# Optimization experiments

Hardware: AMD Instinct MI355X
Metric: run time of the kernel (lower is better)

Reference implementation:

```python
import jax, jax.numpy as jnp
import numpy as np

B, S, HID = 2, 2048, 1024
NH, HD = 16, 64  # num heads, head dim
NEG = 1e10

def setup_inputs() -> dict:
    key = jax.random.key(0)
    ks = jax.random.split(key, 4)
    scale = 1.0 / np.sqrt(HID)
    return {
        "hidden_states": jax.random.normal(ks[0], (B, S, HID), jnp.float32),
        "attention_mask": jnp.zeros((B, 1, 1, S), jnp.float32),
        "Wq": jax.random.normal(ks[1], (HID, HID), jnp.float32) * scale,
        "bq": jnp.zeros((HID,), jnp.float32),
        "Wk": jax.random.normal(ks[2], (HID, HID), jnp.float32) * scale,
        "bk": jnp.zeros((HID,), jnp.float32),
        "Wv": jax.random.normal(ks[3], (HID, HID), jnp.float32) * scale,
        "bv": jnp.zeros((HID,), jnp.float32),
    }

def _split_heads(x):
    # [B,S,HID] -> [B,NH,S,HD]
    return x.reshape(B, S, NH, HD).transpose(0, 2, 1, 3)

def reference(hidden_states, attention_mask, Wq, bq, Wk, bk, Wv, bv):
    q = _split_heads(hidden_states @ Wq.T + bq)
    k = _split_heads(hidden_states @ Wk.T + bk)
    v = _split_heads(hidden_states @ Wv.T + bv)
    scores = jnp.einsum("bhqd,bhkd->bhqk", q, k) / np.sqrt(HD)
    causal = jnp.tril(jnp.ones((S, S), jnp.float32))  # [S,S]
    scores = scores * causal - NEG * (1.0 - causal)
    scores = scores + attention_mask
    probs = jax.nn.softmax(scores, axis=-1)  # [B,NH,S,S]
    ctx = jnp.einsum("bhqk,bhkd->bhqd", probs, v)
    ctx = ctx.transpose(0, 2, 1, 3).reshape(B, S, HID)
    return (ctx, probs)
```

## Files before the change

kernel.cpp:

```cpp
#include <hip/hip_runtime.h>

#define S_LEN 2048
#define HIDN  1024
#define NHEAD 16
#define HDIM  64
#define NBATCH 2

typedef __bf16 bf16x8 __attribute__((ext_vector_type(8)));
typedef float  f32x4  __attribute__((ext_vector_type(4)));
typedef unsigned int  u32x4 __attribute__((ext_vector_type(4)));
typedef unsigned short u16;
typedef unsigned short u16x4 __attribute__((ext_vector_type(4)));

__device__ __forceinline__ u16 f2bf(float f) {
    union { float f; unsigned int u; } v; v.f = f;
    unsigned int u = v.u;
    unsigned int r = ((u >> 16) & 1u) + 0x7FFFu;
    return (u16)((u + r) >> 16);
}

__device__ __forceinline__ f32x4 mfma16(bf16x8 a, bf16x8 b, f32x4 c) {
    return __builtin_amdgcn_mfma_f32_16x16x32_bf16(a, b, c, 0, 0, 0);
}

__device__ __forceinline__ f32x4 zf4() { f32x4 z = {0.f, 0.f, 0.f, 0.f}; return z; }

__device__ __forceinline__ bf16x8 pack8_trunc(f32x4 a, f32x4 b) {
    union { f32x4 f; u32x4 u; } ua, ub;
    ua.f = a; ub.f = b;
    union { unsigned int d[4]; bf16x8 v; } r;
    r.d[0] = __builtin_amdgcn_perm(ua.u.y, ua.u.x, 0x07060302u);
    r.d[1] = __builtin_amdgcn_perm(ua.u.w, ua.u.z, 0x07060302u);
    r.d[2] = __builtin_amdgcn_perm(ub.u.y, ub.u.x, 0x07060302u);
    r.d[3] = __builtin_amdgcn_perm(ub.u.w, ub.u.z, 0x07060302u);
    return r.v;
}

__device__ __forceinline__ void gld16(void* lds, const void* g) {
    __builtin_amdgcn_global_load_lds(
        (const __attribute__((address_space(1))) void*)g,
        (__attribute__((address_space(3))) void*)lds, 16, 0, 0);
}

__global__ __launch_bounds__(256) void cvt_bf16(
    const float* __restrict__ s, u16* __restrict__ d, int n)
{
    int i = (blockIdx.x * 256 + threadIdx.x) * 4;
    if (i >= n) return;
    float4 v = *(const float4*)&s[i];
    u16x4 o = { f2bf(v.x), f2bf(v.y), f2bf(v.z), f2bf(v.w) };
    *(u16x4*)&d[i] = o;
}

__global__ __launch_bounds__(256) void qkv_gemm(
    const u16* __restrict__ hsb,
    const u16* __restrict__ Wqb, const u16* __restrict__ Wkb, const u16* __restrict__ Wvb,
    const float* __restrict__ bq, const float* __restrict__ bk, const float* __restrict__ bv,
    u16* __restrict__ Qf, u16* __restrict__ Kf, u16* __restrict__ Vt)
{
    __shared__ u16 As[128 * 32];
    __shared__ u16 Bs[128 * 32];

    const int z = blockIdx.z;
    const u16*   __restrict__ W    = (z == 0) ? Wqb : (z == 1) ? Wkb : Wvb;
    const float* __restrict__ bias = (z == 0) ? bq  : (z == 1) ? bk  : bv;

    const int mbase = blockIdx.x * 128;
    const int nbase = blockIdx.y * 128;
    const int tid  = threadIdx.x;
    const int lane = tid & 63;
    const int wv   = tid >> 6;
    const int wrow = wv >> 1, wcol = wv & 1;
    const int lrow = lane & 15, quad = lane >> 4;

    const int c0 = tid, c1 = tid + 256;
    const int r0 = c0 >> 2, o0 = (c0 & 3) * 8;
    const int r1 = c1 >> 2, o1 = (c1 & 3) * 8;
    const u16* a0p = &hsb[(size_t)(mbase + r0) * HIDN + o0];
    const u16* a1p = &hsb[(size_t)(mbase + r1) * HIDN + o1];
    const u16* b0p = &W  [(size_t)(nbase + r0) * HIDN + o0];
    const u16* b1p = &W  [(size_t)(nbase + r1) * HIDN + o1];

    f32x4 acc[4][4];
#pragma unroll
    for (int i = 0; i < 4; ++i)
#pragma unroll
        for (int j = 0; j < 4; ++j) acc[i][j] = zf4();

    for (int k0 = 0; k0 < HIDN; k0 += 32) {
        gld16(&As[c0 * 8], a0p + k0);
        gld16(&As[c1 * 8], a1p + k0);
        gld16(&Bs[c0 * 8], b0p + k0);
        gld16(&Bs[c1 * 8], b1p + k0);
        __syncthreads();

        bf16x8 af[4], bfr[4];
#pragma unroll
        for (int i = 0; i < 4; ++i)
            af[i] = *(const bf16x8*)&As[(wrow * 64 + i * 16 + lrow) * 32 + quad * 8];
#pragma unroll
        for (int j = 0; j < 4; ++j)
            bfr[j] = *(const bf16x8*)&Bs[(wcol * 64 + j * 16 + lrow) * 32 + quad * 8];
#pragma unroll
        for (int i = 0; i < 4; ++i)
#pragma unroll
            for (int j = 0; j < 4; ++j)
                acc[i][j] = mfma16(af[i], bfr[j], acc[i][j]);
        __syncthreads();
    }

    if (z == 2) {
        const int bb = mbase >> 11;
        const int sb = mbase & 2047;
#pragma unroll
        for (int i = 0; i < 4; ++i) {
#pragma unroll
            for (int j = 0; j < 4; ++j) {
                const int n = nbase + wcol * 64 + j * 16 + lrow;
                const int hh = n >> 6, d = n & 63;
                const float bs = bias[n];
                const int sbase = sb + wrow * 64 + i * 16 + quad * 4;
                u16x4 pk = { f2bf(acc[i][j][0] + bs), f2bf(acc[i][j][1] + bs),
                             f2bf(acc[i][j][2] + bs), f2bf(acc[i][j][3] + bs) };
                *(u16x4*)&Vt[(((size_t)(bb * NHEAD + hh)) * HDIM + d) * S_LEN + sbase] = pk;
            }
        }
    } else {
        u16* __restrict__ O = (z == 0) ? Qf : Kf;
#pragma unroll
        for (int i = 0; i < 4; ++i) {
#pragma unroll
            for (int j = 0; j < 4; ++j) {
                const int n = nbase + wcol * 64 + j * 16 + lrow;
                const float bs = bias[n];
#pragma unroll
                for (int reg = 0; reg < 4; ++reg) {
                    const int m = mbase + wrow * 64 + i * 16 + quad * 4 + reg;
                    O[(size_t)m * HIDN + n] = f2bf(acc[i][j][reg] + bs);
                }
            }
        }
    }
}

__global__ __launch_bounds__(256) void attn_kernel(
    const u16* __restrict__ Qf,
    const u16* __restrict__ Kf,
    const u16* __restrict__ Vt,
    const float* __restrict__ amask,
    float* __restrict__ ctx,
    float* __restrict__ probs)
{
    const int qt = 127 - blockIdx.x;
    const int h  = blockIdx.y;
    const int b  = blockIdx.z;
    const int bh = b * NHEAD + h;
    const int tid  = threadIdx.x;
    const int lane = tid & 63;
    const int wv   = tid >> 6;
    const int lrow = lane & 15, quad = lane >> 4;
    const int row0 = qt * 16;
    const int dti  = qt >> 2;
    const int nkt  = dti + 1;

    __shared__ float pfl[4][16 * 64];
    __shared__ float cxs[4][64 * 17];
    __shared__ float l_sh[4][16];

    {
        const int tail  = nkt * 64;
        const int nt4   = (S_LEN - tail) >> 2;
        const int r  = tid >> 4;
        const int c0 = tid & 15;
        const f32x4 zf = {0.f, 0.f, 0.f, 0.f};
        float* pr = &probs[((size_t)bh * S_LEN + row0 + r) * S_LEN + tail];
        for (int c4 = c0; c4 < nt4; c4 += 16)
            __builtin_nontemporal_store(zf, (f32x4*)&pr[c4 * 4]);
    }

    const u16* qp = &Qf[((size_t)b * S_LEN + row0 + lrow) * HIDN + h * HDIM + quad * 8];
    const bf16x8 qa0 = *(const bf16x8*)qp;
    const bf16x8 qa1 = *(const bf16x8*)(qp + 32);

    float l_lane[4] = {0.f, 0.f, 0.f, 0.f};
    for (int kt = wv; kt < nkt; kt += 4) {
        f32x4 c[4];
#pragma unroll
        for (int cb = 0; cb < 4; ++cb) {
            const int col = kt * 64 + cb * 16 + lrow;
            const u16* kp = &Kf[((size_t)b * S_LEN + col) * HIDN + h * HDIM + quad * 8];
            bf16x8 kb0 = *(const bf16x8*)kp;
            bf16x8 kb1 = *(const bf16x8*)(kp + 32);
            c[cb] = mfma16(qa0, kb0, zf4());
            c[cb] = mfma16(qa1, kb1, c[cb]);
        }
        if (kt == dti) {
#pragma unroll
            for (int cb = 0; cb < 4; ++cb) {
                const int col = kt * 64 + cb * 16 + lrow;
                const float m8 = amask[b * S_LEN + col] - 8.0f;
#pragma unroll
                for (int reg = 0; reg < 4; ++reg) {
                    const int row = row0 + quad * 4 + reg;
                    const float e = __expf(fmaf(c[cb][reg], 0.125f, m8));
                    l_lane[reg] += (col <= row) ? e : 0.f;
                }
            }
        } else {
#pragma unroll
            for (int cb = 0; cb < 4; ++cb) {
                const int col = kt * 64 + cb * 16 + lrow;
                const float m8 = amask[b * S_LEN + col] - 8.0f;
#pragma unroll
                for (int reg = 0; reg < 4; ++reg)
                    l_lane[reg] += __expf(fmaf(c[cb][reg], 0.125f, m8));
            }
        }
    }
#pragma unroll
    for (int reg = 0; reg < 4; ++reg) {
#pragma unroll
        for (int off = 1; off < 16; off <<= 1)
            l_lane[reg] += __shfl_xor(l_lane[reg], off, 16);
    }
    if (lrow == 0) {
#pragma unroll
        for (int reg = 0; reg < 4; ++reg)
            l_sh[wv][quad * 4 + reg] = l_lane[reg];
    }
    __syncthreads();
    float inv_l[4];
#pragma unroll
    for (int reg = 0; reg < 4; ++reg) {
        const int rr = quad * 4 + reg;
        inv_l[reg] = 1.f / (l_sh[0][rr] + l_sh[1][rr] + l_sh[2][rr] + l_sh[3][rr]);
    }

    f32x4 av[4];
#pragma unroll
    for (int db = 0; db < 4; ++db) av[db] = zf4();

    for (int kt = wv; kt < nkt; kt += 4) {
        f32x4 c[4];
#pragma unroll
        for (int cb = 0; cb < 4; ++cb) {
            const int col = kt * 64 + cb * 16 + lrow;
            const u16* kp = &Kf[((size_t)b * S_LEN + col) * HIDN + h * HDIM + quad * 8];
            bf16x8 kb0 = *(const bf16x8*)kp;
            bf16x8 kb1 = *(const bf16x8*)(kp + 32);
            c[cb] = mfma16(qa0, kb0, zf4());
            c[cb] = mfma16(qa1, kb1, c[cb]);
        }
        if (kt == dti) {
#pragma unroll
            for (int cb = 0; cb < 4; ++cb) {
                const int col = kt * 64 + cb * 16 + lrow;
                const float m8 = amask[b * S_LEN + col] - 8.0f;
#pragma unroll
                for (int reg = 0; reg < 4; ++reg) {
                    const int row = row0 + quad * 4 + reg;
                    const float p = (col <= row)
                        ? __expf(fmaf(c[cb][reg], 0.125f, m8)) * inv_l[reg] : 0.f;
                    pfl[wv][(quad * 4 + reg) * 64 + cb * 16 + lrow] = p;
                }
            }
        } else {
#pragma unroll
            for (int cb = 0; cb < 4; ++cb) {
                const int col = kt * 64 + cb * 16 + lrow;
                const float m8 = amask[b * S_LEN + col] - 8.0f;
#pragma unroll
                for (int reg = 0; reg < 4; ++reg) {
                    const float p = __expf(fmaf(c[cb][reg], 0.125f, m8)) * inv_l[reg];
                    pfl[wv][(quad * 4 + reg) * 64 + cb * 16 + lrow] = p;
                }
            }
        }

#pragma unroll
        for (int it = 0; it < 4; ++it) {
            const int r  = it * 4 + quad;
            const int f4 = lrow;
            f32x4 v = *(const f32x4*)&pfl[wv][r * 64 + f4 * 4];
            __builtin_nontemporal_store(
                v, (f32x4*)&probs[((size_t)bh * S_LEN + row0 + r) * S_LEN + kt * 64 + f4 * 4]);
        }

        f32x4 p0 = *(const f32x4*)&pfl[wv][lrow * 64 + quad * 8];
        f32x4 p1 = *(const f32x4*)&pfl[wv][lrow * 64 + quad * 8 + 4];
        f32x4 p2 = *(const f32x4*)&pfl[wv][lrow * 64 + 32 + quad * 8];
        f32x4 p3 = *(const f32x4*)&pfl[wv][lrow * 64 + 32 + quad * 8 + 4];
        bf16x8 pa0 = pack8_trunc(p0, p1);
        bf16x8 pa1 = pack8_trunc(p2, p3);
#pragma unroll
        for (int db = 0; db < 4; ++db) {
            const u16* vp = &Vt[((size_t)bh * HDIM + db * 16 + lrow) * S_LEN + kt * 64 + quad * 8];
            bf16x8 vb0 = *(const bf16x8*)vp;
            bf16x8 vb1 = *(const bf16x8*)(vp + 32);
            av[db] = mfma16(pa0, vb0, av[db]);
            av[db] = mfma16(pa1, vb1, av[db]);
        }
    }

#pragma unroll
    for (int db = 0; db < 4; ++db)
#pragma unroll
        for (int reg = 0; reg < 4; ++reg)
            cxs[wv][lane * 17 + db * 4 + reg] = av[db][reg];
    __syncthreads();
#pragma unroll
    for (int reg = 0; reg < 4; ++reg) {
        const int idx = lane * 17 + wv * 4 + reg;
        const float s = cxs[0][idx] + cxs[1][idx] + cxs[2][idx] + cxs[3][idx];
        __builtin_nontemporal_store(
            s, &ctx[((size_t)b * S_LEN + row0 + quad * 4 + reg) * HIDN + h * HDIM + wv * 16 + lrow]);
    }
}

extern "C" void kernel_launch(void* const* d_in, const int* in_sizes, int n_in,
                              void* d_out, int out_size, void* d_ws, size_t ws_size,
                              hipStream_t stream)
{
    const float* hs    = (const float*)d_in[0];
    const float* amask = (const float*)d_in[1];
    const float* Wq    = (const float*)d_in[2];
    const float* bq    = (const float*)d_in[3];
    const float* Wk    = (const float*)d_in[4];
    const float* bk    = (const float*)d_in[5];
    const float* Wv    = (const float*)d_in[6];
    const float* bv    = (const float*)d_in[7];

    float* out   = (float*)d_out;
    float* ctx   = out;
    float* probs = out + (size_t)NBATCH * S_LEN * HIDN;

    const size_t NTOK = (size_t)NBATCH * S_LEN;
    u16* hsb = (u16*)d_ws;
    u16* Wqb = hsb + NTOK * HIDN;
    u16* Wkb = Wqb + (size_t)HIDN * HIDN;
    u16* Wvb = Wkb + (size_t)HIDN * HIDN;
    u16* Qf  = Wvb + (size_t)HIDN * HIDN;
    u16* Kf  = Qf + NTOK * HIDN;
    u16* Vt  = Kf + NTOK * HIDN;

    const int n_hs = (int)(NTOK * HIDN);
    const int n_w  = HIDN * HIDN;
    cvt_bf16<<<n_hs / 1024, 256, 0, stream>>>(hs, hsb, n_hs);
    cvt_bf16<<<n_w  / 1024, 256, 0, stream>>>(Wq, Wqb, n_w);
    cvt_bf16<<<n_w  / 1024, 256, 0, stream>>>(Wk, Wkb, n_w);
    cvt_bf16<<<n_w  / 1024, 256, 0, stream>>>(Wv, Wvb, n_w);

    qkv_gemm<<<dim3(32, 8, 3), 256, 0, stream>>>(hsb, Wqb, Wkb, Wvb, bq, bk, bv, Qf, Kf, Vt);
    attn_kernel<<<dim3(128, 16, 2), 256, 0, stream>>>(Qf, Kf, Vt, amask, ctx, probs);
}
```

Before: 778.3 us.

## Give each wave its own 16-row query tile over all key tiles, dropping cross-wave reduction

The attention block now covers 64 query rows, with each of the 4 waves owning 16 rows and looping over every key tile. Before, 4 waves split the key tiles of one 16-row tile. This removes the shared-memory row-sum and context reductions and both __syncthreads, and cuts the grid from 128 to 32 blocks per head. The exponentials also switch to exp2f with log2e folded into the scale constants. The trade-offs are fewer blocks, uneven per-wave work, and waves reading the same K/V tiles separately instead of sharing them.

```diff
diff --git a/kernel.cpp b/kernel.cpp
--- a/kernel.cpp
+++ b/kernel.cpp
@@ -11,6 +11,10 @@
 typedef unsigned int  u32x4 __attribute__((ext_vector_type(4)));
 typedef unsigned short u16;
 typedef unsigned short u16x4 __attribute__((ext_vector_type(4)));
+
+#define LOG2E      1.4426950408889634f
+#define QS_L2E     0.18033688011112042f
+#define NEG8_L2E  -11.541560327111707f
 
 __device__ __forceinline__ u16 f2bf(float f) {
     union { float f; unsigned int u; } v; v.f = f;
@@ -151,7 +155,7 @@
     float* __restrict__ ctx,
     float* __restrict__ probs)
 {
-    const int qt = 127 - blockIdx.x;
+    const int qt = 31 - blockIdx.x;
     const int h  = blockIdx.y;
     const int b  = blockIdx.z;
     const int bh = b * NHEAD + h;
@@ -159,22 +163,19 @@
     const int lane = tid & 63;
     const int wv   = tid >> 6;
     const int lrow = lane & 15, quad = lane >> 4;
-    const int row0 = qt * 16;
-    const int dti  = qt >> 2;
-    const int nkt  = dti + 1;
+    const int nkt  = qt + 1;
+    const int row0 = qt * 64 + wv * 16;
 
     __shared__ float pfl[4][16 * 64];
-    __shared__ float cxs[4][64 * 17];
-    __shared__ float l_sh[4][16];
 
     {
-        const int tail  = nkt * 64;
-        const int nt4   = (S_LEN - tail) >> 2;
-        const int r  = tid >> 4;
-        const int c0 = tid & 15;
+        const int tail = nkt * 64;
+        const int nt4  = (S_LEN - tail) >> 2;
+        const int r  = tid >> 2;
+        const int c0 = tid & 3;
         const f32x4 zf = {0.f, 0.f, 0.f, 0.f};
-        float* pr = &probs[((size_t)bh * S_LEN + row0 + r) * S_LEN + tail];
-        for (int c4 = c0; c4 < nt4; c4 += 16)
+        float* pr = &probs[((size_t)bh * S_LEN + qt * 64 + r) * S_LEN + tail];
+        for (int c4 = c0; c4 < nt4; c4 += 4)
             __builtin_nontemporal_store(zf, (f32x4*)&pr[c4 * 4]);
     }
 
@@ -182,27 +183,30 @@
     const bf16x8 qa0 = *(const bf16x8*)qp;
     const bf16x8 qa1 = *(const bf16x8*)(qp + 32);
 
+    const float* __restrict__ am = &amask[(size_t)b * S_LEN];
+    const u16* __restrict__ kbase = &Kf[(size_t)b * S_LEN * HIDN + h * HDIM + quad * 8];
+
     float l_lane[4] = {0.f, 0.f, 0.f, 0.f};
-    for (int kt = wv; kt < nkt; kt += 4) {
+    for (int kt = 0; kt < nkt; ++kt) {
         f32x4 c[4];
 #pragma unroll
         for (int cb = 0; cb < 4; ++cb) {
             const int col = kt * 64 + cb * 16 + lrow;
-            const u16* kp = &Kf[((size_t)b * S_LEN + col) * HIDN + h * HDIM + quad * 8];
+            const u16* kp = kbase + (size_t)col * HIDN;
             bf16x8 kb0 = *(const bf16x8*)kp;
             bf16x8 kb1 = *(const bf16x8*)(kp + 32);
             c[cb] = mfma16(qa0, kb0, zf4());
             c[cb] = mfma16(qa1, kb1, c[cb]);
         }
-        if (kt == dti) {
+        if (kt == qt) {
 #pragma unroll
             for (int cb = 0; cb < 4; ++cb) {
                 const int col = kt * 64 + cb * 16 + lrow;
-                const float m8 = amask[b * S_LEN + col] - 8.0f;
+                const float m8 = fmaf(am[col], LOG2E, NEG8_L2E);
 #pragma unroll
                 for (int reg = 0; reg < 4; ++reg) {
                     const int row = row0 + quad * 4 + reg;
-                    const float e = __expf(fmaf(c[cb][reg], 0.125f, m8));
+                    const float e = exp2f(fmaf(c[cb][reg], QS_L2E, m8));
                     l_lane[reg] += (col <= row) ? e : 0.f;
                 }
             }
@@ -210,91 +214,83 @@
 #pragma unroll
             for (int cb = 0; cb < 4; ++cb) {
                 const int col = kt * 64 + cb * 16 + lrow;
-                const float m8 = amask[b * S_LEN + col] - 8.0f;
+                const float m8 = fmaf(am[col], LOG2E, NEG8_L2E);
 #pragma unroll
                 for (int reg = 0; reg < 4; ++reg)
-                    l_lane[reg] += __expf(fmaf(c[cb][reg], 0.125f, m8));
-            }
-        }
-    }
+                    l_lane[reg] += exp2f(fmaf(c[cb][reg], QS_L2E, m8));
+            }
+        }
+    }
+    float inv_l[4];
 #pragma unroll
     for (int reg = 0; reg < 4; ++reg) {
 #pragma unroll
         for (int off = 1; off < 16; off <<= 1)
             l_lane[reg] += __shfl_xor(l_lane[reg], off, 16);
-    }
-    if (lrow == 0) {
-#pragma unroll
-        for (int reg = 0; reg < 4; ++reg)
-            l_sh[wv][quad * 4 + reg] = l_lane[reg];
-    }
-    __syncthreads();
-    float inv_l[4];
-#pragma unroll
-    for (int reg = 0; reg < 4; ++reg) {
-        const int rr = quad * 4 + reg;
-        inv_l[reg] = 1.f / (l_sh[0][rr] + l_sh[1][rr] + l_sh[2][rr] + l_sh[3][rr]);
+        inv_l[reg] = 1.f / l_lane[reg];
     }
 
     f32x4 av[4];
 #pragma unroll
     for (int db = 0; db < 4; ++db) av[db] = zf4();
 
-    for (int kt = wv; kt < nkt; kt += 4) {
+    float* __restrict__ pw = pfl[wv];
+    const u16* __restrict__ vbase = &Vt[(size_t)bh * HDIM * S_LEN + quad * 8];
+
+    for (int kt = 0; kt < nkt; ++kt) {
         f32x4 c[4];
 #pragma unroll
         for (int cb = 0; cb < 4; ++cb) {
             const int col = kt * 64 + cb * 16 + lrow;
-            const u16* kp = &Kf[((size_t)b * S_LEN + col) * HIDN + h * HDIM + quad * 8];
+            const u16* kp = kbase + (size_t)col * HIDN;
             bf16x8 kb0 = *(const bf16x8*)kp;
             bf16x8 kb1 = *(const bf16x8*)(kp + 32);
             c[cb] = mfma16(qa0, kb0, zf4());
             c[cb] = mfma16(qa1, kb1, c[cb]);
         }
-        if (kt == dti) {
+        if (kt == qt) {
 #pragma unroll
             for (int cb = 0; cb < 4; ++cb) {
                 const int col = kt * 64 + cb * 16 + lrow;
-                const float m8 = amask[b * S_LEN + col] - 8.0f;
+                const float m8 = fmaf(am[col], LOG2E, NEG8_L2E);
 #pragma unroll
                 for (int reg = 0; reg < 4; ++reg) {
                     const int row = row0 + quad * 4 + reg;
                     const float p = (col <= row)
-                        ? __expf(fmaf(c[cb][reg], 0.125f, m8)) * inv_l[reg] : 0.f;
-                    pfl[wv][(quad * 4 + reg) * 64 + cb * 16 + lrow] = p;
+                        ? exp2f(fmaf(c[cb][reg], QS_L2E, m8)) * inv_l[reg] : 0.f;
+                    pw[(quad * 4 + reg) * 64 + cb * 16 + lrow] = p;
                 }
             }
         } else {
 #pragma unroll
             for (int cb = 0; cb < 4; ++cb) {
                 const int col = kt * 64 + cb * 16 + lrow;
-                const float m8 = amask[b * S_LEN + col] - 8.0f;
+                const float m8 = fmaf(am[col], LOG2E, NEG8_L2E);
 #pragma unroll
                 for (int reg = 0; reg < 4; ++reg) {
-                    const float p = __expf(fmaf(c[cb][reg], 0.125f, m8)) * inv_l[reg];
-                    pfl[wv][(quad * 4 + reg) * 64 + cb * 16 + lrow] = p;
+                    const float p = exp2f(fmaf(c[cb][reg], QS_L2E, m8)) * inv_l[reg];
+                    pw[(quad * 4 + reg) * 64 + cb * 16 + lrow] = p;
                 }
             }
         }
 
 #pragma unroll
         for (int it = 0; it < 4; ++it) {
-            const int r  = it * 4 + quad;
-            const int f4 = lrow;
-            f32x4 v = *(const f32x4*)&pfl[wv][r * 64 + f4 * 4];
+            const int r = it * 4 + quad;
+            f32x4 v = *(const f32x4*)&pw[r * 64 + lrow * 4];
             __builtin_nontemporal_store(
-                v, (f32x4*)&probs[((size_t)bh * S_LEN + row0 + r) * S_LEN + kt * 64 + f4 * 4]);
-        }
-
-        f32x4 p0 = *(const f32x4*)&pfl[wv][lrow * 64 + quad * 8];
-        f32x4 p1 = *(const f32x4*)&pfl[wv][lrow * 64 + quad * 8 + 4];
-        f32x4 p2 = *(const f32x4*)&pfl[wv][lrow * 64 + 32 + quad * 8];
-        f32x4 p3 = *(const f32x4*)&pfl[wv][lrow * 64 + 32 + quad * 8 + 4];
+                v, (f32x4*)&probs[((size_t)bh * S_LEN + row0 + r) * S_LEN + kt * 64 + lrow * 4]);
+        }
+
+        f32x4 p0 = *(const f32x4*)&pw[lrow * 64 + quad * 8];
+        f32x4 p1 = *(const f32x4*)&pw[lrow * 64 + quad * 8 + 4];
+        f32x4 p2 = *(const f32x4*)&pw[lrow * 64 + 32 + quad * 8];
+        f32x4 p3 = *(const f32x4*)&pw[lrow * 64 + 32 + quad * 8 + 4];
         bf16x8 pa0 = pack8_trunc(p0, p1);
         bf16x8 pa1 = pack8_trunc(p2, p3);
 #pragma unroll
         for (int db = 0; db < 4; ++db) {
-            const u16* vp = &Vt[((size_t)bh * HDIM + db * 16 + lrow) * S_LEN + kt * 64 + quad * 8];
+            const u16* vp = vbase + (size_t)(db * 16 + lrow) * S_LEN + kt * 64;
             bf16x8 vb0 = *(const bf16x8*)vp;
             bf16x8 vb1 = *(const bf16x8*)(vp + 32);
             av[db] = mfma16(pa0, vb0, av[db]);
@@ -303,17 +299,14 @@
     }
 
 #pragma unroll
-    for (int db = 0; db < 4; ++db)
-#pragma unroll
-        for (int reg = 0; reg < 4; ++reg)
-            cxs[wv][lane * 17 + db * 4 + reg] = av[db][reg];
-    __syncthreads();
-#pragma unroll
-    for (int reg = 0; reg < 4; ++reg) {
-        const int idx = lane * 17 + wv * 4 + reg;
-        const float s = cxs[0][idx] + cxs[1][idx] + cxs[2][idx] + cxs[3][idx];
-        __builtin_nontemporal_store(
-            s, &ctx[((size_t)b * S_LEN + row0 + quad * 4 + reg) * HIDN + h * HDIM + wv * 16 + lrow]);
+    for (int db = 0; db < 4; ++db) {
+#pragma unroll
+        for (int reg = 0; reg < 4; ++reg) {
+            __builtin_nontemporal_store(
+                av[db][reg],
+                &ctx[((size_t)b * S_LEN + row0 + quad * 4 + reg) * HIDN
+                     + h * HDIM + db * 16 + lrow]);
+        }
     }
 }
 
@@ -351,5 +344,5 @@
     cvt_bf16<<<n_w  / 1024, 256, 0, stream>>>(Wv, Wvb, n_w);
 
     qkv_gemm<<<dim3(32, 8, 3), 256, 0, stream>>>(hsb, Wqb, Wkb, Wvb, bq, bk, bv, Qf, Kf, Vt);
-    attn_kernel<<<dim3(128, 16, 2), 256, 0, stream>>>(Qf, Kf, Vt, amask, ctx, probs);
-}
+    attn_kernel<<<dim3(32, 16, 2), 256, 0, stream>>>(Qf, Kf, Vt, amask, ctx, probs);
+}
```

Result: slower. 924.7 us (+18.8%).
